# Kernel tuning notes

Measured on AMD Instinct MI355X. Metric: run time of the kernel, lower is better.

## Reference

```python
import jax, jax.numpy as jnp
import numpy as np

EPS = 1e-6
D, L, HEADS, FF = 384, 12, 6, 1536


def _ln(x, w, b):
    m = x.mean(-1, keepdims=True)
    v = ((x - m) ** 2).mean(-1, keepdims=True)
    return (x - m) / jnp.sqrt(v + EPS) * w + b


def setup_inputs() -> dict:
    key = jax.random.key(0)
    ks = iter(jax.random.split(key, 16))
    B, Cin, H, W = 16, 7, 192, 640
    N = (H // 16) * (W // 16) + 1  # 481 tokens

    def w(shape, s=0.02):
        return (jax.random.normal(next(ks), shape, jnp.float32) * s)

    return dict(
        input=jax.random.normal(next(ks), (B, Cin, H, W), jnp.float32),
        conv_w=w((D, Cin, 16, 16)),
        conv_b=jnp.zeros((D,), jnp.float32),
        cls_token=w((1, 1, D)),
        pos_embed=w((1, N, D)),
        ln1_w=jnp.ones((L, D), jnp.float32), ln1_b=jnp.zeros((L, D), jnp.float32),
        qkv_w=w((L, 3 * D, D)), qkv_b=jnp.zeros((L, 3 * D), jnp.float32),
        proj_w=w((L, D, D)), proj_b=jnp.zeros((L, D), jnp.float32),
        ln2_w=jnp.ones((L, D), jnp.float32), ln2_b=jnp.zeros((L, D), jnp.float32),
        fc1_w=w((L, FF, D)), fc1_b=jnp.zeros((L, FF), jnp.float32),
        fc2_w=w((L, D, FF)), fc2_b=jnp.zeros((L, D), jnp.float32),
        norm_w=jnp.ones((D,), jnp.float32), norm_b=jnp.zeros((D,), jnp.float32),
        to_qkv_w=w((3 * D, D)),
        pose_w=w((D, D)), pose_b=jnp.zeros((D,), jnp.float32),
    )


def reference(input, conv_w, conv_b, cls_token, pos_embed, ln1_w, ln1_b,
              qkv_w, qkv_b, proj_w, proj_b, ln2_w, ln2_b, fc1_w, fc1_b,
              fc2_w, fc2_b, norm_w, norm_b, to_qkv_w, pose_w, pose_b):
    B = input.shape[0]
    dh = D // HEADS
    # patch embed: conv stride=kernel=16 -> [B,384,12,40] -> [B,480,384]
    x = jax.lax.conv_general_dilated(
        input, conv_w, (16, 16), 'VALID',
        dimension_numbers=('NCHW', 'OIHW', 'NCHW')) + conv_b[None, :, None, None]
    x = x.reshape(B, D, -1).transpose(0, 2, 1)
    x = jnp.concatenate([jnp.broadcast_to(cls_token, (B, 1, D)), x], axis=1) + pos_embed
    # 12 pre-norm ViT blocks (timm vit_small: 6 heads, GELU, eps=1e-6)
    for i in range(L):
        h = _ln(x, ln1_w[i], ln1_b[i])
        qkv = h @ qkv_w[i].T + qkv_b[i]
        q, k, v = jnp.split(qkv, 3, axis=-1)
        hd = lambda t: t.reshape(B, -1, HEADS, dh).transpose(0, 2, 1, 3)
        q, k, v = hd(q) * (dh ** -0.5), hd(k), hd(v)
        a = jax.nn.softmax(jnp.einsum('bhqd,bhkd->bhqk', q, k), axis=-1)
        o = jnp.einsum('bhqk,bhkd->bhqd', a, v).transpose(0, 2, 1, 3).reshape(B, -1, D)
        x = x + o @ proj_w[i].T + proj_b[i]
        h = _ln(x, ln2_w[i], ln2_b[i])
        h = jax.nn.gelu(h @ fc1_w[i].T + fc1_b[i], approximate=False)
        x = x + h @ fc2_w[i].T + fc2_b[i]
    x = _ln(x, norm_w, norm_b)
    # ---- make_pose (training branch: per-column-chunk softmax + median mask) ----
    t = x[:, 1:, :]                      # drop cls -> [B,480,384]
    N = t.shape[1]
    qkv = (t @ to_qkv_w.T).reshape(B, N, 3, D).transpose(2, 0, 1, 3)
    q, k, v = qkv[0] * 0.05103, qkv[1], qkv[2]
    attn = jnp.einsum('bqc,bkc->bqk', q, k) / 100.0
    # col chunk c = columns {c + 40*j : j=0..11}; 40 disjoint chunks of 12
    col_idx = jnp.arange(40)[:, None] + 40 * jnp.arange(12)[None, :]  # [40,12]
    part = jax.nn.softmax(attn[:, :, col_idx], axis=-1)               # [B,N,40,12]
    # torch.median of 12 values = lower median = sorted index (12-1)//2
    med = jnp.sort(part, axis=-1)[..., (12 - 1) // 2][..., None]
    mask = jnp.where(part > med, 0.0, part)
    flat_cols = col_idx.reshape(-1)  # permutation of 0..479
    attn_new = jnp.zeros_like(attn).at[:, :, flat_cols].set(part.reshape(B, N, N))
    masked = jnp.zeros_like(attn).at[:, :, flat_cols].set(mask.reshape(B, N, N))
    masked = masked / ((D // 8) / 2)  # /= num_indices/2 = 24
    # NOTE: einsum 'bal,bnc->bac' shares only 'b': rowsum(attn) outer rowsum(v)
    out = jnp.einsum('bal,bnc->bac', attn_new, v)
    out = out @ pose_w.T + pose_b
    out = _ln(out, norm_w, norm_b)
    attn_map = attn_new.mean(axis=1).reshape(B, 12, 40)
    masked_map = masked.mean(axis=1).reshape(B, 12, 40)
    return out.mean(axis=1), attn_map, masked_map
```

## Files before the change

kernel.cpp:

```cpp
#include <hip/hip_runtime.h>
#include <hip/hip_bf16.h>

#define TD 384
#define NHEAD 6
#define NFF 1536
#define NB 16
#define NTOK 481
#define NROWS (NB*NTOK)
#define MPAD 7744

typedef __attribute__((ext_vector_type(8))) __bf16 bf16x8;
typedef __attribute__((ext_vector_type(4))) __bf16 bf16x4;
typedef __attribute__((ext_vector_type(4))) float f32x4;

static __device__ __forceinline__ float gelu_f(float v){
    return 0.5f*v*(1.0f + erff(v*0.70710678118654752f));
}

static __device__ __forceinline__ void gload16(const void* g, void* l){
    __builtin_amdgcn_global_load_lds((const __attribute__((address_space(1))) void*)g,
                                     (__attribute__((address_space(3))) void*)l, 16, 0, 0);
}

template<int ROWS>
static __device__ __forceinline__ void stageT(const __bf16* g, int ldel, __bf16* lds, int w, int lane){
    #pragma unroll
    for (int j = 0; j < ROWS/32; ++j){
        int i = w*(ROWS/32) + j;
        int ol = i*1024 + lane*16;
        int row = ol >> 7, colb = ol & 127;
        int sc = colb ^ ((row & 7) << 4);
        gload16((const char*)g + (long)row*ldel*2 + sc, (char*)lds + i*1024);
    }
}

__global__ __launch_bounds__(256) void mgemm(
    const __bf16* __restrict__ A, int lda, long sA,
    const __bf16* __restrict__ Bm, int ldb, long sB,
    void* __restrict__ Cp, int ldc, long sC,
    const float* __restrict__ bias,
    const float* __restrict__ Rp, long sR,
    int M, int N, int K, float scale, int act, int obf)
{
    __shared__ __align__(16) __bf16 As[2][64*64];
    __shared__ __align__(16) __bf16 Bs[2][128*64];
    const int bz = blockIdx.z;
    A  += (long)bz*sA; Bm += (long)bz*sB;

    const int nwg = gridDim.x*gridDim.y;
    const int id  = blockIdx.y*gridDim.x + blockIdx.x;
    const int q8  = nwg >> 3, r8 = nwg & 7;
    const int xcd = id & 7, sub = id >> 3;
    const int nid = (xcd < r8 ? xcd*(q8+1) : r8*(q8+1) + (xcd-r8)*q8) + sub;
    const int m0 = (nid / gridDim.x) * 64, n0 = (nid % gridDim.x) * 128;

    const int tid = threadIdx.x;
    const int w = tid >> 6, lane = tid & 63;
    const int wr = w >> 1, wc = w & 1;
    const int lr = lane & 15, lg = lane >> 4;

    f32x4 acc[2][4];
    #pragma unroll
    for (int m=0;m<2;++m)
        #pragma unroll
        for (int n=0;n<4;++n)
            acc[m][n] = (f32x4){0.f,0.f,0.f,0.f};

    const __bf16* Ag = A + (long)m0*lda;
    const __bf16* Bg = Bm + (long)n0*ldb;
    const int NT = K >> 6;

    stageT<64>(Ag, lda, As[0], w, lane);
    stageT<128>(Bg, ldb, Bs[0], w, lane);
    int cur = 0;
    for (int t = 0; t < NT; ++t){
        if (t+1 < NT){
            stageT<64>(Ag + (t+1)*64, lda, As[cur^1], w, lane);
            stageT<128>(Bg + (t+1)*64, ldb, Bs[cur^1], w, lane);
            asm volatile("s_waitcnt vmcnt(6)" ::: "memory");
        } else {
            asm volatile("s_waitcnt vmcnt(0)" ::: "memory");
        }
        __builtin_amdgcn_sched_barrier(0);
        __builtin_amdgcn_s_barrier();
        #pragma unroll
        for (int kk=0;kk<2;++kk){
            const int sa = ((kk*64 + lg*16) ^ ((lr&7)<<4));
            bf16x8 af[2], bfr[4];
            #pragma unroll
            for (int m=0;m<2;++m)
                af[m] = *(const bf16x8*)((const char*)&As[cur][0] + (wr*32 + m*16 + lr)*128 + sa);
            #pragma unroll
            for (int n=0;n<4;++n)
                bfr[n] = *(const bf16x8*)((const char*)&Bs[cur][0] + (wc*64 + n*16 + lr)*128 + sa);
            #pragma unroll
            for (int m=0;m<2;++m)
                #pragma unroll
                for (int n=0;n<4;++n)
                    acc[m][n] = __builtin_amdgcn_mfma_f32_16x16x32_bf16(af[m], bfr[n], acc[m][n], 0, 0, 0);
        }
        __builtin_amdgcn_s_barrier();
        cur ^= 1;
    }

    #pragma unroll
    for (int m=0;m<2;++m){
        #pragma unroll
        for (int n=0;n<4;++n){
            int col = n0 + wc*64 + n*16 + lr;
            if (col >= N) continue;
            #pragma unroll
            for (int e=0;e<4;++e){
                int row = m0 + wr*32 + m*16 + lg*4 + e;
                if (row >= M) continue;
                float v = acc[m][n][e]*scale;
                if (bias) v += bias[col];
                if (act) v = gelu_f(v);
                if (Rp) v += Rp[(long)bz*sR + (long)row*ldc + col];
                if (obf) ((__bf16*)Cp)[(long)bz*sC + (long)row*ldc + col] = (__bf16)v;
                else     ((float*)Cp)[(long)bz*sC + (long)row*ldc + col] = v;
            }
        }
    }
}

__global__ __launch_bounds__(256) void attn2(const __bf16* __restrict__ QKV, __bf16* __restrict__ O)
{
    __shared__ __align__(16) __bf16 Ks[64*64];
    __shared__ __align__(16) __bf16 VT[64*72];
    __shared__ __align__(16) __bf16 Ps[64*72];
    const int qt=blockIdx.x, h=blockIdx.y, b=blockIdx.z;
    const int tid=threadIdx.x, w=tid>>6, lane=tid&63;
    const int lr=lane&15, lg=lane>>4;
    const __bf16* base = QKV + (long)b*NTOK*1152;
    const long qrow = qt*64 + w*16 + lr;
    const bf16x8 qa0 = *(const bf16x8*)(base + qrow*1152 + h*64 + lg*8);
    const bf16x8 qa1 = *(const bf16x8*)(base + qrow*1152 + h*64 + 32 + lg*8);

    f32x4 oacc[4];
    float mo[4], lo[4];
    #pragma unroll
    for (int e=0;e<4;++e){ mo[e]=-1e30f; lo[e]=0.f; }
    #pragma unroll
    for (int n=0;n<4;++n) oacc[n]=(f32x4){0.f,0.f,0.f,0.f};

    for (int kt=0; kt<8; ++kt){
        __syncthreads();
        #pragma unroll
        for (int j=0;j<2;++j){
            int i = w*2+j;
            int ol = i*1024 + lane*16;
            int row = ol>>7, colb = ol&127;
            int sc = colb ^ ((row&7)<<4);
            gload16((const char*)base + ((long)(kt*64+row)*1152 + 384 + h*64)*2 + sc,
                    (char*)Ks + i*1024);
        }
        #pragma unroll
        for (int rep=0;rep<2;++rep){
            int c = tid + rep*256;
            int kv = c & 63, d8 = c >> 6;
            bf16x8 vv = *(const bf16x8*)(base + (long)(kt*64+kv)*1152 + 768 + h*64 + d8*8);
            #pragma unroll
            for (int jj=0;jj<8;++jj) VT[(d8*8+jj)*72 + kv] = vv[jj];
        }
        __syncthreads();

        f32x4 s[4];
        #pragma unroll
        for (int n=0;n<4;++n) s[n]=(f32x4){0.f,0.f,0.f,0.f};
        #pragma unroll
        for (int kk=0;kk<2;++kk){
            const int sa = ((kk*64 + lg*16) ^ ((lr&7)<<4));
            #pragma unroll
            for (int n=0;n<4;++n){
                bf16x8 kb = *(const bf16x8*)((const char*)Ks + (n*16+lr)*128 + sa);
                s[n] = __builtin_amdgcn_mfma_f32_16x16x32_bf16(kk? qa1:qa0, kb, s[n], 0,0,0);
            }
        }
        #pragma unroll
        for (int n=0;n<4;++n){
            int col = kt*64 + n*16 + lr;
            bool bad = col >= NTOK;
            #pragma unroll
            for (int e=0;e<4;++e) s[n][e] = bad ? -1e30f : s[n][e]*0.125f;
        }
        #pragma unroll
        for (int e=0;e<4;++e){
            float rm = fmaxf(fmaxf(s[0][e],s[1][e]), fmaxf(s[2][e],s[3][e]));
            rm = fmaxf(rm, __shfl_xor(rm,1));
            rm = fmaxf(rm, __shfl_xor(rm,2));
            rm = fmaxf(rm, __shfl_xor(rm,4));
            rm = fmaxf(rm, __shfl_xor(rm,8));
            float mn = fmaxf(mo[e], rm);
            float al = __expf(mo[e]-mn);
            float rs = 0.f;
            #pragma unroll
            for (int n=0;n<4;++n){ float p=__expf(s[n][e]-mn); s[n][e]=p; rs+=p; }
            rs += __shfl_xor(rs,1); rs += __shfl_xor(rs,2);
            rs += __shfl_xor(rs,4); rs += __shfl_xor(rs,8);
            lo[e] = lo[e]*al + rs; mo[e]=mn;
            #pragma unroll
            for (int n=0;n<4;++n) oacc[n][e] *= al;
        }
        #pragma unroll
        for (int n=0;n<4;++n)
            #pragma unroll
            for (int e=0;e<4;++e)
                Ps[(w*16+lg*4+e)*72 + n*16+lr] = (__bf16)s[n][e];
        #pragma unroll
        for (int kk=0;kk<2;++kk){
            bf16x8 pa = *(const bf16x8*)&Ps[(w*16+lr)*72 + kk*32 + lg*8];
            #pragma unroll
            for (int n=0;n<4;++n){
                bf16x8 vf = *(const bf16x8*)&VT[(n*16+lr)*72 + kk*32 + lg*8];
                oacc[n] = __builtin_amdgcn_mfma_f32_16x16x32_bf16(pa, vf, oacc[n], 0,0,0);
            }
        }
    }
    #pragma unroll
    for (int e=0;e<4;++e){
        int q = qt*64 + w*16 + lg*4 + e;
        if (q < NTOK){
            float inv = 1.f/lo[e];
            __bf16* op = O + ((long)b*NTOK + q)*TD + h*64;
            #pragma unroll
            for (int n=0;n<4;++n)
                op[n*16+lr] = (__bf16)(oacc[n][e]*inv);
        }
    }
}

__global__ __launch_bounds__(128) void ln_kernel(const float* __restrict__ Xp, __bf16* __restrict__ Y,
    const float* __restrict__ W, const float* __restrict__ Bp)
{
    long r = blockIdx.x;
    int t = threadIdx.x;
    const float* x = Xp + r*TD;
    float v0 = x[t], v1 = x[t+128], v2 = x[t+256];
    float s = v0+v1+v2;
    float q = v0*v0+v1*v1+v2*v2;
    #pragma unroll
    for (int w=1; w<64; w<<=1){ s += __shfl_xor(s,w); q += __shfl_xor(q,w); }
    __shared__ float sm[2][2];
    if ((t&63)==0){ sm[t>>6][0]=s; sm[t>>6][1]=q; }
    __syncthreads();
    float S = sm[0][0]+sm[1][0];
    float Q = sm[0][1]+sm[1][1];
    float mean = S*(1.f/384.f);
    float var  = Q*(1.f/384.f) - mean*mean;
    float rstd = rsqrtf(var + 1e-6f);
    __bf16* y = Y + r*TD;
    y[t]     = (__bf16)((v0-mean)*rstd*W[t]     + Bp[t]);
    y[t+128] = (__bf16)((v1-mean)*rstd*W[t+128] + Bp[t+128]);
    y[t+256] = (__bf16)((v2-mean)*rstd*W[t+256] + Bp[t+256]);
}

__global__ void wconv_kernel(const float* __restrict__ s, __bf16* __restrict__ d, int n4){
    int i = blockIdx.x*256 + threadIdx.x;
    if (i < n4){
        float4 v = ((const float4*)s)[i];
        bf16x4 p; p[0]=(__bf16)v.x; p[1]=(__bf16)v.y; p[2]=(__bf16)v.z; p[3]=(__bf16)v.w;
        ((bf16x4*)d)[i] = p;
    }
}

__global__ void im2col_kernel(const float* __restrict__ in, __bf16* __restrict__ outp)
{
    long idx = (long)blockIdx.x*256 + threadIdx.x;
    if (idx >= (long)7680*1792) return;
    int k = (int)(idx % 1792);
    long m = idx / 1792;
    int pw = (int)(m % 40);
    long t2 = m / 40;
    int ph = (int)(t2 % 12);
    int b  = (int)(t2 / 12);
    int kw = k & 15, kh = (k >> 4) & 15, c = k >> 8;
    outp[idx] = (__bf16)in[(((long)(b*7 + c)*192) + ph*16 + kh)*640 + pw*16 + kw];
}

__global__ void assemble_kernel(const float* __restrict__ CO, const float* __restrict__ cls,
    const float* __restrict__ pos, float* __restrict__ X)
{
    long idx = (long)blockIdx.x*256 + threadIdx.x;
    if (idx >= (long)NROWS*TD) return;
    int d = (int)(idx % TD);
    long r = idx / TD;
    int tok = (int)(r % NTOK);
    int b   = (int)(r / NTOK);
    float v = (tok == 0) ? cls[d] : CO[((long)b*480 + tok-1)*TD + d];
    X[idx] = v + pos[tok*TD + d];
}

__global__ __launch_bounds__(256) void pose_maps_kernel(const float* __restrict__ PA,
    float* __restrict__ attn_map, float* __restrict__ masked_map)
{
    int i = blockIdx.x;
    int b = blockIdx.y;
    int t = threadIdx.x;
    float accA[12], accM[12];
    #pragma unroll
    for (int j=0;j<12;++j){ accA[j]=0.f; accM[j]=0.f; }
    for (int a = t; a < 480; a += 256) {
        const float* row = PA + ((long)(b*480 + a))*480 + i;
        float v[12];
        float mx = -1e30f;
        #pragma unroll
        for (int j=0;j<12;++j){ v[j] = row[40*j]; mx = fmaxf(mx, v[j]); }
        float sum = 0.f;
        #pragma unroll
        for (int j=0;j<12;++j){ v[j] = expf(v[j]-mx); sum += v[j]; }
        float invs = 1.f/sum;
        #pragma unroll
        for (int j=0;j<12;++j) v[j] *= invs;
        float srt[12];
        #pragma unroll
        for (int j=0;j<12;++j){
            float x = v[j]; int p = j;
            while (p > 0 && srt[p-1] > x){ srt[p]=srt[p-1]; --p; }
            srt[p]=x;
        }
        float med = srt[5];
        #pragma unroll
        for (int j=0;j<12;++j){
            accA[j] += v[j];
            accM[j] += (v[j] > med) ? 0.f : v[j];
        }
    }
    __shared__ float redA[256*12];
    __shared__ float redM[256*12];
    #pragma unroll
    for (int j=0;j<12;++j){ redA[t*12+j]=accA[j]; redM[t*12+j]=accM[j]; }
    __syncthreads();
    for (int sgap=128; sgap>0; sgap>>=1){
        if (t < sgap){
            #pragma unroll
            for (int j=0;j<12;++j){
                redA[t*12+j] += redA[(t+sgap)*12+j];
                redM[t*12+j] += redM[(t+sgap)*12+j];
            }
        }
        __syncthreads();
    }
    if (t < 12){
        attn_map  [(b*12 + t)*40 + i] = redA[t] * (1.f/480.f);
        masked_map[(b*12 + t)*40 + i] = redM[t] * (1.f/480.f) * (1.f/24.f);
    }
}

__global__ __launch_bounds__(384) void colsum4_kernel(const __bf16* __restrict__ QKV2, float* __restrict__ CS4)
{
    int b = blockIdx.x, j = blockIdx.y, c = threadIdx.x;
    const __bf16* p = QKV2 + (long)b*480*1152 + 768 + c;
    float s = 0.f;
    for (int a = j*120; a < j*120+120; ++a) s += (float)p[(long)a*1152];
    CS4[((long)b*4 + j)*384 + c] = s;
}

__global__ __launch_bounds__(384) void pose_final_kernel(const float* __restrict__ CS4,
    const float* __restrict__ PW, const float* __restrict__ PB,
    const float* __restrict__ NW, const float* __restrict__ NBb, float* __restrict__ out)
{
    int b = blockIdx.x, c = threadIdx.x;
    const float* s0 = CS4 + (long)b*1536;
    __shared__ float sv[384];
    sv[c] = s0[c] + s0[384+c] + s0[768+c] + s0[1152+c];
    __syncthreads();
    const float* wr = PW + (long)c*384;
    float acc = 0.f;
    for (int k = 0; k < 384; ++k) acc += sv[k]*wr[k];
    acc = 40.f*acc + PB[c];
    float s = acc, q = acc*acc;
    #pragma unroll
    for (int w=1; w<64; w<<=1){ s += __shfl_xor(s,w); q += __shfl_xor(q,w); }
    __shared__ float sm[6][2];
    if ((c & 63) == 0){ sm[c>>6][0]=s; sm[c>>6][1]=q; }
    __syncthreads();
    float S=0.f, Q=0.f;
    for (int i=0;i<6;++i){ S+=sm[i][0]; Q+=sm[i][1]; }
    float mean = S*(1.f/384.f);
    float var  = Q*(1.f/384.f) - mean*mean;
    float rstd = rsqrtf(var + 1e-6f);
    out[b*384 + c] = (acc-mean)*rstd*NW[c] + NBb[c];
}

extern "C" void kernel_launch(void* const* d_in, const int* in_sizes, int n_in,
                              void* d_out, int out_size, void* d_ws, size_t ws_size,
                              hipStream_t stream)
{
    const float* input  = (const float*)d_in[0];
    const float* conv_w = (const float*)d_in[1];
    const float* conv_b = (const float*)d_in[2];
    const float* cls    = (const float*)d_in[3];
    const float* pos    = (const float*)d_in[4];
    const float* ln1w   = (const float*)d_in[5];
    const float* ln1b   = (const float*)d_in[6];
    const float* qkvw   = (const float*)d_in[7];
    const float* qkvb   = (const float*)d_in[8];
    const float* projw  = (const float*)d_in[9];
    const float* projb  = (const float*)d_in[10];
    const float* ln2w   = (const float*)d_in[11];
    const float* ln2b   = (const float*)d_in[12];
    const float* fc1w   = (const float*)d_in[13];
    const float* fc1b   = (const float*)d_in[14];
    const float* fc2w   = (const float*)d_in[15];
    const float* fc2b   = (const float*)d_in[16];
    const float* normw  = (const float*)d_in[17];
    const float* normb  = (const float*)d_in[18];
    const float* toqkvw = (const float*)d_in[19];
    const float* posew  = (const float*)d_in[20];
    const float* poseb  = (const float*)d_in[21];
    float* out = (float*)d_out;
    float* ws  = (float*)d_ws;

    __bf16* WB   = (__bf16*)ws;
    float*  X    = ws + 11182080;
    __bf16* Hbf  = (__bf16*)(ws + 11182080 + 2955264);
    __bf16* QKVb = (__bf16*)(ws + 11182080 + 2955264 + 1486848);
    __bf16* Obuf = (__bf16*)(ws + 11182080 + 2955264 + 1486848 + 5947392);
    float*  PAb  = ws + 23058432;
    float*  CS4  = PAb + 3686400;
    __bf16* IM2C = QKVb;

    __bf16* Wconv = WB;
    __bf16* Wqkv  = WB + 688128;
    __bf16* Wproj = WB + 5996544;
    __bf16* Wfc1  = WB + 7766016;
    __bf16* Wfc2  = WB + 14843904;
    __bf16* Wtoq  = WB + 21921792;

    wconv_kernel<<<dim3((172032+255)/256), 256, 0, stream>>>(conv_w, Wconv, 172032);
    wconv_kernel<<<dim3((1327104+255)/256), 256, 0, stream>>>(qkvw,  Wqkv, 1327104);
    wconv_kernel<<<dim3((442368+255)/256), 256, 0, stream>>>(projw, Wproj, 442368);
    wconv_kernel<<<dim3((1769472+255)/256), 256, 0, stream>>>(fc1w,  Wfc1, 1769472);
    wconv_kernel<<<dim3((1769472+255)/256), 256, 0, stream>>>(fc2w,  Wfc2, 1769472);
    wconv_kernel<<<dim3((110592+255)/256), 256, 0, stream>>>(toqkvw, Wtoq, 110592);

    {
        long total = (long)7680*1792;
        im2col_kernel<<<dim3((unsigned)((total+255)/256)), 256, 0, stream>>>(input, IM2C);
    }
    mgemm<<<dim3(3, 120, 1), 256, 0, stream>>>(IM2C, 1792, 0, Wconv, 1792, 0,
        PAb, 384, 0, conv_b, nullptr, 0, 7680, 384, 1792, 1.f, 0, 0);
    assemble_kernel<<<dim3((NROWS*TD+255)/256), 256, 0, stream>>>(PAb, cls, pos, X);

    for (int i = 0; i < 12; ++i) {
        ln_kernel<<<dim3(NROWS), 128, 0, stream>>>(X, Hbf, ln1w + i*384, ln1b + i*384);
        mgemm<<<dim3(9, 121, 1), 256, 0, stream>>>(Hbf, 384, 0, Wqkv + (long)i*1152*384, 384, 0,
            QKVb, 1152, 0, qkvb + i*1152, nullptr, 0, NROWS, 1152, 384, 1.f, 0, 1);
        attn2<<<dim3(8, NHEAD, NB), 256, 0, stream>>>(QKVb, Obuf);
        mgemm<<<dim3(3, 121, 1), 256, 0, stream>>>(Obuf, 384, 0, Wproj + (long)i*384*384, 384, 0,
            X, 384, 0, projb + i*384, X, 0, NROWS, 384, 384, 1.f, 0, 0);
        ln_kernel<<<dim3(NROWS), 128, 0, stream>>>(X, Hbf, ln2w + i*384, ln2b + i*384);
        mgemm<<<dim3(12, 121, 1), 256, 0, stream>>>(Hbf, 384, 0, Wfc1 + (long)i*1536*384, 384, 0,
            QKVb, 1536, 0, fc1b + i*1536, nullptr, 0, NROWS, 1536, 384, 1.f, 1, 1);
        mgemm<<<dim3(3, 121, 1), 256, 0, stream>>>(QKVb, 1536, 0, Wfc2 + (long)i*384*1536, 1536, 0,
            X, 384, 0, fc2b + i*384, X, 0, NROWS, 384, 1536, 1.f, 0, 0);
    }
    ln_kernel<<<dim3(NROWS), 128, 0, stream>>>(X, Hbf, normw, normb);

    mgemm<<<dim3(9, 8, 16), 256, 0, stream>>>(Hbf + 384, 384, (long)481*384,
        Wtoq, 384, 0, QKVb, 1152, (long)480*1152, nullptr, nullptr, 0, 480, 1152, 384, 1.f, 0, 1);
    mgemm<<<dim3(4, 8, 16), 256, 0, stream>>>(QKVb, 1152, (long)480*1152,
        QKVb + 384, 1152, (long)480*1152, PAb, 480, (long)480*480, nullptr, nullptr, 0,
        480, 480, 384, 0.05103f*0.01f, 0, 0);
    pose_maps_kernel<<<dim3(40, 16), 256, 0, stream>>>(PAb, out + 6144, out + 13824);
    colsum4_kernel<<<dim3(16, 4), 384, 0, stream>>>(QKVb, CS4);
    pose_final_kernel<<<dim3(16), 384, 0, stream>>>(CS4, posew, poseb, normw, normb, out);
}
```

Before: 2.114 ms.

## Triple-buffer GEMM LDS staging with prefetch distance two and a single barrier

Moves the bf16 MFMA GEMM from double to triple LDS buffering. Global-to-LDS loads for tile t+2 are issued right after the per-iteration barrier, which removes the trailing barrier. All fragment reads for both k-halves are hoisted ahead of the MFMA chain, and wave priority is raised during the MFMAs. Workspace offsets are shifted to give the intermediate buffers more room. In exchange, LDS use per block rises by half and more registers hold fragments, which may lower occupancy.

```diff
diff --git a/kernel.cpp b/kernel.cpp
--- a/kernel.cpp
+++ b/kernel.cpp
@@ -7,7 +7,6 @@
 #define NB 16
 #define NTOK 481
 #define NROWS (NB*NTOK)
-#define MPAD 7744
 
 typedef __attribute__((ext_vector_type(8))) __bf16 bf16x8;
 typedef __attribute__((ext_vector_type(4))) __bf16 bf16x4;
@@ -42,8 +41,8 @@
     const float* __restrict__ Rp, long sR,
     int M, int N, int K, float scale, int act, int obf)
 {
-    __shared__ __align__(16) __bf16 As[2][64*64];
-    __shared__ __align__(16) __bf16 Bs[2][128*64];
+    __shared__ __align__(16) __bf16 As[3][64*64];
+    __shared__ __align__(16) __bf16 Bs[3][128*64];
     const int bz = blockIdx.z;
     A  += (long)bz*sA; Bm += (long)bz*sB;
 
@@ -70,37 +69,44 @@
     const __bf16* Bg = Bm + (long)n0*ldb;
     const int NT = K >> 6;
 
-    stageT<64>(Ag, lda, As[0], w, lane);
-    stageT<128>(Bg, ldb, Bs[0], w, lane);
-    int cur = 0;
+    stageT<64>(Ag,        lda, As[0], w, lane);
+    stageT<128>(Bg,       ldb, Bs[0], w, lane);
+    stageT<64>(Ag + 64,   lda, As[1], w, lane);
+    stageT<128>(Bg + 64,  ldb, Bs[1], w, lane);
+
     for (int t = 0; t < NT; ++t){
-        if (t+1 < NT){
-            stageT<64>(Ag + (t+1)*64, lda, As[cur^1], w, lane);
-            stageT<128>(Bg + (t+1)*64, ldb, Bs[cur^1], w, lane);
-            asm volatile("s_waitcnt vmcnt(6)" ::: "memory");
-        } else {
-            asm volatile("s_waitcnt vmcnt(0)" ::: "memory");
-        }
+        if (t+1 < NT) asm volatile("s_waitcnt vmcnt(6)" ::: "memory");
+        else          asm volatile("s_waitcnt vmcnt(0)" ::: "memory");
         __builtin_amdgcn_sched_barrier(0);
         __builtin_amdgcn_s_barrier();
+        if (t+2 < NT){
+            stageT<64>(Ag + (t+2)*64,  lda, As[(t+2)%3], w, lane);
+            stageT<128>(Bg + (t+2)*64, ldb, Bs[(t+2)%3], w, lane);
+        }
+        const __bf16* Ac = As[t%3];
+        const __bf16* Bc = Bs[t%3];
+        bf16x8 af[2][2], bfr[2][4];
         #pragma unroll
         for (int kk=0;kk<2;++kk){
             const int sa = ((kk*64 + lg*16) ^ ((lr&7)<<4));
-            bf16x8 af[2], bfr[4];
             #pragma unroll
             for (int m=0;m<2;++m)
-                af[m] = *(const bf16x8*)((const char*)&As[cur][0] + (wr*32 + m*16 + lr)*128 + sa);
+                af[kk][m] = *(const bf16x8*)((const char*)Ac + (wr*32 + m*16 + lr)*128 + sa);
             #pragma unroll
             for (int n=0;n<4;++n)
-                bfr[n] = *(const bf16x8*)((const char*)&Bs[cur][0] + (wc*64 + n*16 + lr)*128 + sa);
+                bfr[kk][n] = *(const bf16x8*)((const char*)Bc + (wc*64 + n*16 + lr)*128 + sa);
+        }
+        asm volatile("s_waitcnt lgkmcnt(0)" ::: "memory");
+        __builtin_amdgcn_sched_barrier(0);
+        __builtin_amdgcn_s_setprio(1);
+        #pragma unroll
+        for (int kk=0;kk<2;++kk)
             #pragma unroll
             for (int m=0;m<2;++m)
                 #pragma unroll
                 for (int n=0;n<4;++n)
-                    acc[m][n] = __builtin_amdgcn_mfma_f32_16x16x32_bf16(af[m], bfr[n], acc[m][n], 0, 0, 0);
-        }
-        __builtin_amdgcn_s_barrier();
-        cur ^= 1;
+                    acc[m][n] = __builtin_amdgcn_mfma_f32_16x16x32_bf16(af[kk][m], bfr[kk][n], acc[m][n], 0, 0, 0);
+        __builtin_amdgcn_s_setprio(0);
     }
 
     #pragma unroll
@@ -414,10 +420,10 @@
 
     __bf16* WB   = (__bf16*)ws;
     float*  X    = ws + 11182080;
-    __bf16* Hbf  = (__bf16*)(ws + 11182080 + 2955264);
-    __bf16* QKVb = (__bf16*)(ws + 11182080 + 2955264 + 1486848);
-    __bf16* Obuf = (__bf16*)(ws + 11182080 + 2955264 + 1486848 + 5947392);
-    float*  PAb  = ws + 23058432;
+    __bf16* Hbf  = (__bf16*)(ws + 14137344);
+    __bf16* QKVb = (__bf16*)(ws + 15636480);
+    __bf16* Obuf = (__bf16*)(ws + 21633024);
+    float*  PAb  = ws + 23132160;
     float*  CS4  = PAb + 3686400;
     __bf16* IM2C = QKVb;
 
```

New measurement: 2.415 ms. +14.3%, slower.
